# Kernel optimization log

Measured on AMD Instinct MI355X. Metric: run time of the kernel, lower is better.

Reference implementation:

```python
import jax, jax.numpy as jnp
import numpy as np

N = 20000   # nodes
E = 256000  # edges
G = 64      # graphs
EPS = 1e-5  # batchnorm eps


def setup_inputs() -> dict:
    key = jax.random.key(0)
    ks = jax.random.split(key, 20)
    inp = {}
    inp['x'] = jax.random.normal(ks[0], (N, 6), dtype=jnp.float32)
    inp['edge_index'] = jax.random.randint(ks[1], (2, E), 0, N)
    inp['batch'] = jnp.sort(jax.random.randint(ks[2], (N,), 0, G))
    conv_dims = [(6, 32), (32, 64), (64, 128), (128, 1024)]
    ki = 3
    for li, (a, b) in enumerate(conv_dims, 1):
        inp[f'W{li}'] = jax.random.normal(ks[ki], (a, b), dtype=jnp.float32) / np.sqrt(a).astype(np.float32); ki += 1
        inp[f'b{li}'] = jnp.zeros((b,), jnp.float32)
        inp[f'g{li}'] = jnp.ones((b,), jnp.float32)
        inp[f'be{li}'] = jnp.zeros((b,), jnp.float32)
    fc_dims = [(1024, 512), (512, 256), (256, 64)]
    for li, (a, b) in enumerate(fc_dims, 5):
        inp[f'W{li}'] = jax.random.normal(ks[ki], (a, b), dtype=jnp.float32) / np.sqrt(a).astype(np.float32); ki += 1
        inp[f'b{li}'] = jnp.zeros((b,), jnp.float32)
        if li < 7:
            inp[f'g{li}'] = jnp.ones((b,), jnp.float32)
            inp[f'be{li}'] = jnp.zeros((b,), jnp.float32)
    return inp


def _bn(h, g, be):
    # training-mode BatchNorm1d: biased variance over dim 0
    m = h.mean(axis=0)
    v = h.var(axis=0)
    return g * (h - m) * jax.lax.rsqrt(v + EPS) + be


def reference(x, edge_index, batch,
              W1, b1, g1, be1, W2, b2, g2, be2,
              W3, b3, g3, be3, W4, b4, g4, be4,
              W5, b5, g5, be5, W6, b6, g6, be6,
              W7, b7):
    loops = jnp.arange(N)
    src = jnp.concatenate([edge_index[0], loops])  # [E+N], message sources
    dst = jnp.concatenate([edge_index[1], loops])  # [E+N], aggregation targets
    deg = jax.ops.segment_sum(jnp.ones(E + N, x.dtype), dst, num_segments=N)
    dinv = jax.lax.rsqrt(deg)                      # deg >= 1 (self-loops)
    norm = dinv[src] * dinv[dst]                   # symmetric GCN normalization

    def gcn(h, W, b):
        h = h @ W                                   # [N, out]
        agg = jax.ops.segment_sum(norm[:, None] * h[src], dst, num_segments=N)
        return agg + b

    h = jax.nn.relu(_bn(gcn(x, W1, b1), g1, be1))
    h = jax.nn.relu(_bn(gcn(h, W2, b2), g2, be2))
    h = jax.nn.relu(_bn(gcn(h, W3, b3), g3, be3))
    h = jax.nn.relu(_bn(gcn(h, W4, b4), g4, be4))
    p = jax.ops.segment_max(h, batch, num_segments=G)  # global max pool [G, 1024]
    p = jax.nn.relu(_bn(p @ W5 + b5, g5, be5))
    p = jax.nn.relu(_bn(p @ W6 + b6, g6, be6))
    y = p @ W7 + b7
    n = jnp.maximum(jnp.linalg.norm(y, axis=1, keepdims=True), 1e-12)
    return y / n
```

## Files before the change

### kernel.cpp

```cpp
#include <hip/hip_runtime.h>
#include <math.h>

#define NN 20000
#define EE 256000
#define GG 64
#define CDIV(a,b) (((a)+(b)-1)/(b))

typedef __attribute__((ext_vector_type(8))) short bf16x8;
typedef __attribute__((ext_vector_type(4))) float f32x4;

__device__ __forceinline__ unsigned fkey(float f) {
  unsigned u = __float_as_uint(f);
  return (u & 0x80000000u) ? ~u : (u | 0x80000000u);
}
__device__ __forceinline__ float fdec(unsigned k) {
  unsigned u = (k & 0x80000000u) ? (k ^ 0x80000000u) : ~k;
  return __uint_as_float(u);
}
__device__ __forceinline__ unsigned short rne_bf16(float f) {
  unsigned u = __float_as_uint(f);
  unsigned r = (u + 0x7fffu + ((u >> 16) & 1u)) >> 16;
  return (unsigned short)r;
}


__global__ void k_prep(int* deg) {
  int i = blockIdx.x*blockDim.x + threadIdx.x;
  if (i < NN) deg[i] = 1;
}

__global__ void k_deg(const int* __restrict__ dst, int* deg) {
  int i = blockIdx.x*blockDim.x + threadIdx.x;
  if (i < EE) atomicAdd(&deg[dst[i]], 1);
}

__global__ __launch_bounds__(256) void k_scan_bsum(const int* __restrict__ deg,
                                                   int* __restrict__ bsum) {
  __shared__ int red[256];
  int b = blockIdx.x, t = threadIdx.x;
  int idx = b*1024 + t*4;
  int4 v = make_int4(0,0,0,0);
  if (idx < NN) v = *(const int4*)&deg[idx];
  red[t] = v.x + v.y + v.z + v.w;
  __syncthreads();
  for (int off = 128; off > 0; off >>= 1) {
    if (t < off) red[t] += red[t+off];
    __syncthreads();
  }
  if (t == 0) bsum[b] = red[0];
}

__global__ __launch_bounds__(256) void k_scan_apply(
    const int* __restrict__ deg, const int* __restrict__ bsum,
    int* __restrict__ offsets, int* __restrict__ cursor, float* __restrict__ dinv) {
  __shared__ int base_s;
  __shared__ int tsum[256];
  int b = blockIdx.x, t = threadIdx.x;
  if (t == 0) {
    int s = 0;
    for (int i = 0; i < b; ++i) s += bsum[i];
    base_s = s;
  }
  int idx = b*1024 + t*4;
  int4 v = make_int4(0,0,0,0);
  if (idx < NN) v = *(const int4*)&deg[idx];
  tsum[t] = v.x + v.y + v.z + v.w;
  __syncthreads();
  for (int off = 1; off < 256; off <<= 1) {
    int u = (t >= off) ? tsum[t-off] : 0;
    __syncthreads();
    tsum[t] += u;
    __syncthreads();
  }
  int excl = (t == 0) ? 0 : tsum[t-1];
  if (idx < NN) {
    int base = base_s + excl;
    int o0 = base;
    int o1 = o0 + v.x;
    int o2 = o1 + v.y;
    int o3 = o2 + v.z;
    *(int4*)&offsets[idx] = make_int4(o0,o1,o2,o3);
    *(int4*)&cursor[idx]  = make_int4(o0,o1,o2,o3);
    float4 dv;
    dv.x = rsqrtf((float)v.x); dv.y = rsqrtf((float)v.y);
    dv.z = rsqrtf((float)v.z); dv.w = rsqrtf((float)v.w);
    *(float4*)&dinv[idx] = dv;
    if (idx + 4 == NN) offsets[NN] = o3 + v.w;
  }
}

__global__ void k_fill(const int* __restrict__ srcv, const int* __restrict__ dstv,
                       const float* __restrict__ dinv, int* cursor,
                       int* __restrict__ csr_src, float* __restrict__ csr_w) {
  int i = blockIdx.x*blockDim.x + threadIdx.x;
  if (i < EE) {
    int s = srcv[i], d = dstv[i];
    int pos = atomicAdd(&cursor[d], 1);
    csr_src[pos] = s;
    csr_w[pos] = dinv[s] * dinv[d];
  } else if (i < EE + NN) {
    int n = i - EE;
    int pos = atomicAdd(&cursor[n], 1);
    csr_src[pos] = n;
    float di = dinv[n];
    csr_w[pos] = di * di;
  }
}


template<int C, int TX, int TY>
__global__ void k_agg(const float* __restrict__ in, const int* __restrict__ offsets,
                      const int* __restrict__ csr_src, const float* __restrict__ csr_w,
                      float* __restrict__ out) {
  int node = blockIdx.x * TY + threadIdx.y;
  if (node >= NN) return;
  int x = threadIdx.x;
  int k0 = offsets[node], k1 = offsets[node+1];
  if (x < C) {
    float acc = 0.f;
    for (int k = k0; k < k1; ++k) {
      int s = csr_src[k];
      float w = csr_w[k];
      acc += w * in[s*C + x];
    }
    out[node*C + x] = acc;
  }
}

template<int C, int TY>
__global__ void k_agg_f4(const float* __restrict__ in, const float* __restrict__ st,
                         const float* __restrict__ g, const float* __restrict__ be,
                         const int* __restrict__ offsets, const int* __restrict__ csr_src,
                         const float* __restrict__ csr_w, float* __restrict__ out) {
  int node = blockIdx.x*TY + threadIdx.y;
  if (node >= NN) return;
  int c0 = threadIdx.x*4;
  float4 mean = *(const float4*)&st[c0];
  float4 rstd = *(const float4*)&st[C+c0];
  float4 gv = *(const float4*)&g[c0];
  float4 bv = *(const float4*)&be[c0];
  float sx = gv.x*rstd.x, hx = bv.x - mean.x*sx;
  float sy = gv.y*rstd.y, hy = bv.y - mean.y*sy;
  float sz = gv.z*rstd.z, hz = bv.z - mean.z*sz;
  float sw = gv.w*rstd.w, hw = bv.w - mean.w*sw;
  int k0 = offsets[node], k1 = offsets[node+1];
  float a0=0.f,a1=0.f,a2=0.f,a3=0.f;
  for (int k = k0; k < k1; ++k) {
    int s = csr_src[k]; float w = csr_w[k];
    float4 v = *(const float4*)&in[s*C + c0];
    a0 += w*fmaxf(v.x*sx+hx, 0.f);
    a1 += w*fmaxf(v.y*sy+hy, 0.f);
    a2 += w*fmaxf(v.z*sz+hz, 0.f);
    a3 += w*fmaxf(v.w*sw+hw, 0.f);
  }
  *(float4*)&out[node*C+c0] = make_float4(a0,a1,a2,a3);
}

__global__ void k_agg_bf_f4(const float* __restrict__ in, const float* __restrict__ st,
                            const float* __restrict__ g, const float* __restrict__ be,
                            const int* __restrict__ offsets, const int* __restrict__ csr_src,
                            const float* __restrict__ csr_w, unsigned short* __restrict__ out) {
  int node = blockIdx.x*8 + threadIdx.y;
  if (node >= NN) return;
  int c0 = threadIdx.x*4;
  float4 mean = *(const float4*)&st[c0];
  float4 rstd = *(const float4*)&st[128+c0];
  float4 gv = *(const float4*)&g[c0];
  float4 bv = *(const float4*)&be[c0];
  float sx = gv.x*rstd.x, hx = bv.x - mean.x*sx;
  float sy = gv.y*rstd.y, hy = bv.y - mean.y*sy;
  float sz = gv.z*rstd.z, hz = bv.z - mean.z*sz;
  float sw = gv.w*rstd.w, hw = bv.w - mean.w*sw;
  int k0 = offsets[node], k1 = offsets[node+1];
  float a0=0.f,a1=0.f,a2=0.f,a3=0.f;
  for (int k = k0; k < k1; ++k) {
    int s = csr_src[k]; float w = csr_w[k];
    float4 v = *(const float4*)&in[s*128 + c0];
    a0 += w*fmaxf(v.x*sx+hx, 0.f);
    a1 += w*fmaxf(v.y*sy+hy, 0.f);
    a2 += w*fmaxf(v.z*sz+hz, 0.f);
    a3 += w*fmaxf(v.w*sw+hw, 0.f);
  }
  ushort4 o;
  o.x = rne_bf16(a0); o.y = rne_bf16(a1); o.z = rne_bf16(a2); o.w = rne_bf16(a3);
  *(ushort4*)&out[node*128 + c0] = o;
}

__global__ void k_wprep(const float* __restrict__ W, unsigned short* __restrict__ out) {
  int i = blockIdx.x*256 + threadIdx.x;
  if (i >= 128*1024) return;
  int k = i >> 10, c = i & 1023;
  out[c*128 + k] = rne_bf16(W[i]);
}


template<int K, int OUT, int ROWS>
__global__ __launch_bounds__(256) void k_gemm_small(
    const float* __restrict__ A, const float* __restrict__ W,
    float* __restrict__ out, float* __restrict__ pstats) {
  constexpr int RG  = 256 / OUT;
  constexpr int RPT = ROWS / RG;
  __shared__ float Ws[K*OUT];
  __shared__ float As[ROWS*K];
  __shared__ float reds[2][RG][OUT];
  int t = threadIdx.x;
  for (int i = t; i < K*OUT; i += 256) Ws[i] = W[i];
  int row0 = blockIdx.x * ROWS;
  for (int i = t; i < ROWS*K; i += 256) As[i] = A[row0*K + i];
  __syncthreads();
  int j  = t % OUT;
  int rg = t / OUT;
  float acc[RPT] = {};
  for (int k = 0; k < K; ++k) {
    float w = Ws[k*OUT + j];
    #pragma unroll
    for (int i = 0; i < RPT; ++i)
      acc[i] += As[(rg*RPT + i)*K + k] * w;
  }
  float s = 0.f, ss = 0.f;
  #pragma unroll
  for (int i = 0; i < RPT; ++i) {
    out[(row0 + rg*RPT + i)*OUT + j] = acc[i];
    s += acc[i]; ss += acc[i]*acc[i];
  }
  reds[0][rg][j] = s; reds[1][rg][j] = ss;
  __syncthreads();
  if (rg == 0) {
    float S = 0.f, SS = 0.f;
    #pragma unroll
    for (int r = 0; r < RG; ++r) { S += reds[0][r][j]; SS += reds[1][r][j]; }
    int p = blockIdx.x & 15;
    atomicAdd(&pstats[p*2*OUT + j], S);
    atomicAdd(&pstats[p*2*OUT + OUT + j], SS);
  }
}

template<int C>
__global__ void k_finalize_ps(const float* __restrict__ pstats, float* __restrict__ stats) {
  int c = blockIdx.x*64 + threadIdx.x;
  if (c >= C) return;
  float s = 0.f, ss = 0.f;
  #pragma unroll
  for (int p = 0; p < 16; ++p) { s += pstats[p*2*C + c]; ss += pstats[p*2*C + C + c]; }
  float m = s * (1.f/NN);
  float v = ss * (1.f/NN) - m*m;
  stats[c] = m;
  stats[C+c] = rsqrtf(v + 1e-5f);
}


__global__ __launch_bounds__(256) void k_gemm_l4_mfma(
    const unsigned short* __restrict__ A, const unsigned short* __restrict__ Bt,
    const int* __restrict__ batch,
    float* __restrict__ stats, unsigned* __restrict__ pmax, unsigned* __restrict__ pmin) {
  __shared__ unsigned short As[128*128];
  __shared__ unsigned short Bs[128*128];
  int t = threadIdx.x;
  int row0 = blockIdx.x * 128;
  int col0 = blockIdx.y * 128;
  #pragma unroll
  for (int j = 0; j < 8; ++j) {
    int c = j*256 + t;
    int r = c >> 4, ck = c & 15;
    int rg = row0 + r;
    ulonglong2 v; v.x = 0; v.y = 0;
    if (rg < NN) v = *(const ulonglong2*)&A[rg*128 + ck*8];
    *(ulonglong2*)&As[r*128 + (ck ^ (r & 7))*8] = v;
  }
  #pragma unroll
  for (int j = 0; j < 8; ++j) {
    int c = j*256 + t;
    int r = c >> 4, ck = c & 15;
    ulonglong2 v = *(const ulonglong2*)&Bt[(col0 + r)*128 + ck*8];
    *(ulonglong2*)&Bs[r*128 + (ck ^ (r & 7))*8] = v;
  }
  __syncthreads();

  int w = t >> 6, l = t & 63;
  int wr = w >> 1, wc = w & 1;
  int lrow = l & 15, lk = l >> 4;
  f32x4 acc[4][4] = {};
  #pragma unroll
  for (int ks = 0; ks < 4; ++ks) {
    int kc = ks*4 + lk;
    bf16x8 a[4], b[4];
    #pragma unroll
    for (int m = 0; m < 4; ++m) {
      int r = wr*64 + m*16 + lrow;
      a[m] = *(const bf16x8*)&As[r*128 + (kc ^ (r & 7))*8];
    }
    #pragma unroll
    for (int n = 0; n < 4; ++n) {
      int r = wc*64 + n*16 + lrow;
      b[n] = *(const bf16x8*)&Bs[r*128 + (kc ^ (r & 7))*8];
    }
    #pragma unroll
    for (int m = 0; m < 4; ++m)
      #pragma unroll
      for (int n = 0; n < 4; ++n)
        acc[m][n] = __builtin_amdgcn_mfma_f32_16x16x32_bf16(a[m], b[n], acc[m][n], 0, 0, 0);
  }

  int rbase = row0 + wr*64;
  float s[4] = {}, ss[4] = {};
  float mx[4], mn[4];
  #pragma unroll
  for (int n = 0; n < 4; ++n) { mx[n] = -3.4e38f; mn[n] = 3.4e38f; }
  #pragma unroll
  for (int m = 0; m < 4; ++m)
    #pragma unroll
    for (int r = 0; r < 4; ++r) {
      int row_g = rbase + m*16 + lk*4 + r;
      if (row_g < NN) {
        #pragma unroll
        for (int n = 0; n < 4; ++n) {
          float v = acc[m][n][r];
          s[n] += v; ss[n] += v*v;
          mx[n] = fmaxf(mx[n], v); mn[n] = fminf(mn[n], v);
        }
      }
    }
  #pragma unroll
  for (int n = 0; n < 4; ++n) {
    s[n]  += __shfl_xor(s[n], 16);  s[n]  += __shfl_xor(s[n], 32);
    ss[n] += __shfl_xor(ss[n], 16); ss[n] += __shfl_xor(ss[n], 32);
  }
  if (l < 16) {
    #pragma unroll
    for (int n = 0; n < 4; ++n) {
      int cg = col0 + wc*64 + n*16 + l;
      atomicAdd(&stats[cg], s[n]);
      atomicAdd(&stats[1024 + cg], ss[n]);
    }
  }
  if (rbase < NN) {
    int rlast = min(rbase + 63, NN - 1);
    int glo = batch[rbase], ghi = batch[rlast];
    if (glo == ghi) {
      #pragma unroll
      for (int n = 0; n < 4; ++n) {
        mx[n] = fmaxf(mx[n], __shfl_xor(mx[n], 16)); mx[n] = fmaxf(mx[n], __shfl_xor(mx[n], 32));
        mn[n] = fminf(mn[n], __shfl_xor(mn[n], 16)); mn[n] = fminf(mn[n], __shfl_xor(mn[n], 32));
      }
      if (l < 16) {
        #pragma unroll
        for (int n = 0; n < 4; ++n) {
          int cg = col0 + wc*64 + n*16 + l;
          atomicMax(&pmax[glo*1024 + cg], fkey(mx[n]));
          atomicMin(&pmin[glo*1024 + cg], fkey(mn[n]));
        }
      }
    } else {
      int gb[4][4];
      #pragma unroll
      for (int m = 0; m < 4; ++m)
        #pragma unroll
        for (int r = 0; r < 4; ++r) {
          int row_g = rbase + m*16 + lk*4 + r;
          gb[m][r] = (row_g < NN) ? batch[row_g] : -1;
        }
      for (int g = glo; g <= ghi; ++g) {
        float gmx[4], gmn[4];
        #pragma unroll
        for (int n = 0; n < 4; ++n) { gmx[n] = -3.4e38f; gmn[n] = 3.4e38f; }
        #pragma unroll
        for (int m = 0; m < 4; ++m)
          #pragma unroll
          for (int r = 0; r < 4; ++r) {
            bool in_g = (gb[m][r] == g);
            #pragma unroll
            for (int n = 0; n < 4; ++n) {
              float v = acc[m][n][r];
              gmx[n] = in_g ? fmaxf(gmx[n], v) : gmx[n];
              gmn[n] = in_g ? fminf(gmn[n], v) : gmn[n];
            }
          }
        #pragma unroll
        for (int n = 0; n < 4; ++n) {
          gmx[n] = fmaxf(gmx[n], __shfl_xor(gmx[n], 16)); gmx[n] = fmaxf(gmx[n], __shfl_xor(gmx[n], 32));
          gmn[n] = fminf(gmn[n], __shfl_xor(gmn[n], 16)); gmn[n] = fminf(gmn[n], __shfl_xor(gmn[n], 32));
        }
        if (l < 16) {
          #pragma unroll
          for (int n = 0; n < 4; ++n) {
            int cg = col0 + wc*64 + n*16 + l;
            if (gmx[n] > -3.0e38f) atomicMax(&pmax[g*1024 + cg], fkey(gmx[n]));
            if (gmn[n] <  3.0e38f) atomicMin(&pmin[g*1024 + cg], fkey(gmn[n]));
          }
        }
      }
    }
  }
}

__global__ void k_finalize(float* stats, int C, float invN) {
  int c = blockIdx.x*blockDim.x + threadIdx.x;
  if (c < C) {
    float m = stats[c] * invN;
    float v = stats[C+c]*invN - m*m;
    stats[c] = m;
    stats[C+c] = rsqrtf(v + 1e-5f);
  }
}

__global__ void k_bnpool(const unsigned* __restrict__ pmax, const unsigned* __restrict__ pmin,
                         const float* __restrict__ stats, const float* __restrict__ g,
                         const float* __restrict__ be, float* __restrict__ p) {
  int i = blockIdx.x*256 + threadIdx.x;
  if (i >= 64*1024) return;
  int c = i & 1023;
  float mean = stats[c], rstd = stats[1024+c];
  float sc = g[c]*rstd, sh = be[c] - mean*sc;
  float v = (sc >= 0.f) ? fdec(pmax[i]) : fdec(pmin[i]);
  p[i] = fmaxf(v*sc + sh, 0.f);
}


template<int K, int OUT, int KT>
__global__ __launch_bounds__(256) void k_fc_tile(
    const float* __restrict__ A, const float* __restrict__ W,
    float* __restrict__ out) {
  __shared__ float As[64][KT];
  __shared__ float Ws[KT][64];
  int t = threadIdx.y*64 + threadIdx.x;
  int j0 = blockIdx.x*64;
  int k0 = blockIdx.y*KT;
  #pragma unroll 4
  for (int i = t; i < 64*KT/4; i += 256) {
    int r  = i / (KT/4);
    int c4 = i % (KT/4);
    float4 v = *(const float4*)&A[r*K + k0 + c4*4];
    *(float4*)&As[r][c4*4] = v;
  }
  #pragma unroll 4
  for (int i = t; i < KT*16; i += 256) {
    int k  = i / 16;
    int c4 = i % 16;
    float4 v = *(const float4*)&W[(k0+k)*OUT + j0 + c4*4];
    *(float4*)&Ws[k][c4*4] = v;
  }
  __syncthreads();
  int j  = threadIdx.x;
  int r0 = threadIdx.y*16;
  float acc[16] = {};
  for (int kk = 0; kk < KT; ++kk) {
    float w = Ws[kk][j];
    #pragma unroll
    for (int i = 0; i < 16; ++i) acc[i] += As[r0+i][kk] * w;
  }
  #pragma unroll
  for (int i = 0; i < 16; ++i) atomicAdd(&out[(r0+i)*OUT + j0 + j], acc[i]);
}

__global__ __launch_bounds__(512) void k_bn_rows(
    float* __restrict__ h, const float* __restrict__ g,
    const float* __restrict__ be, int C) {
  int c = blockIdx.x*64 + threadIdx.x;
  int y = threadIdx.y;
  float v[8];
  float s = 0.f, ss = 0.f;
  #pragma unroll
  for (int i = 0; i < 8; ++i) {
    v[i] = h[(y*8+i)*C + c];
    s += v[i]; ss += v[i]*v[i];
  }
  __shared__ float rs[8][64], rss[8][64], bc[2][64];
  rs[y][threadIdx.x] = s; rss[y][threadIdx.x] = ss;
  __syncthreads();
  if (y == 0) {
    s = 0.f; ss = 0.f;
    #pragma unroll
    for (int i = 0; i < 8; ++i) { s += rs[i][threadIdx.x]; ss += rss[i][threadIdx.x]; }
    float m = s*(1.f/64.f);
    float var = ss*(1.f/64.f) - m*m;
    float rstd = rsqrtf(var + 1e-5f);
    float sc = g[c]*rstd;
    bc[0][threadIdx.x] = sc;
    bc[1][threadIdx.x] = be[c] - m*sc;
  }
  __syncthreads();
  float sc = bc[0][threadIdx.x], sh = bc[1][threadIdx.x];
  #pragma unroll
  for (int i = 0; i < 8; ++i)
    h[(y*8+i)*C + c] = fmaxf(v[i]*sc + sh, 0.f);
}

__global__ void k_l2norm(const float* __restrict__ in, const float* __restrict__ b,
                         float* __restrict__ out) {
  int r = blockIdx.x, j = threadIdx.x;
  float v = in[r*64 + j] + b[j];
  float ss = v*v;
  #pragma unroll
  for (int off = 1; off < 64; off <<= 1) ss += __shfl_xor(ss, off);
  float inv = 1.f / fmaxf(sqrtf(ss), 1e-12f);
  out[r*64 + j] = v * inv;
}


extern "C" void kernel_launch(void* const* d_in, const int* in_sizes, int n_in,
                              void* d_out, int out_size, void* d_ws, size_t ws_size,
                              hipStream_t stream) {
  const float* x    = (const float*)d_in[0];
  const int*   ei   = (const int*)d_in[1];
  const int*   batch= (const int*)d_in[2];
  const float* W1=(const float*)d_in[3],  *g1=(const float*)d_in[5],  *be1=(const float*)d_in[6];
  const float* W2=(const float*)d_in[7],  *g2=(const float*)d_in[9],  *be2=(const float*)d_in[10];
  const float* W3=(const float*)d_in[11], *g3=(const float*)d_in[13], *be3=(const float*)d_in[14];
  const float* W4=(const float*)d_in[15], *g4=(const float*)d_in[17], *be4=(const float*)d_in[18];
  const float* W5=(const float*)d_in[19], *g5=(const float*)d_in[21], *be5=(const float*)d_in[22];
  const float* W6=(const float*)d_in[23], *g6=(const float*)d_in[25], *be6=(const float*)d_in[26];
  const float* W7=(const float*)d_in[27], *b7=(const float*)d_in[28];
  const int* esrc = ei;
  const int* edst = ei + EE;

  char* w = (char*)d_ws;
  auto alloc = [&](size_t bytes) -> void* {
    void* p = (void*)w;
    w += (bytes + 255) & ~(size_t)255;
    return p;
  };
  int*   deg     = (int*)  alloc(NN*4);
  int*   offsets = (int*)  alloc((NN+1)*4);
  int*   cursor  = (int*)  alloc(NN*4);
  int*   bsum    = (int*)  alloc(32*4);
  float* dinv    = (float*)alloc(NN*4);
  int*   csr_src = (int*)  alloc((EE+NN)*4);
  float* csr_w   = (float*)alloc((EE+NN)*4);
  float* stats1  = (float*)alloc(2*32*4);
  float* stats2  = (float*)alloc(2*64*4);
  float* stats3  = (float*)alloc(2*128*4);
  float* stats4  = (float*)alloc(2*1024*4);
  float* pstats  = (float*)alloc(16*2*128*4);
  float* agg     = (float*)alloc((size_t)NN*128*4);
  float* hbufA   = (float*)alloc((size_t)NN*128*4);
  float* hbufB   = (float*)alloc((size_t)NN*64*4);
  float* pooled  = (float*)alloc(64*1024*4);
  float* fc1     = (float*)alloc(64*512*4);
  float* fc2     = (float*)alloc(64*256*4);
  float* fc3raw  = (float*)alloc(64*64*4);
  unsigned short* agg_bf = (unsigned short*)alloc((size_t)NN*128*2);
  unsigned short* wt_bf  = (unsigned short*)alloc(1024*128*2);
  unsigned* pmax = (unsigned*)alloc(64*1024*4);
  unsigned* pmin = (unsigned*)alloc(64*1024*4);

  k_prep<<<CDIV(NN,256),256,0,stream>>>(deg);
  k_deg<<<CDIV(EE,256),256,0,stream>>>(edst, deg);
  k_scan_bsum<<<20,256,0,stream>>>(deg, bsum);
  k_scan_apply<<<20,256,0,stream>>>(deg, bsum, offsets, cursor, dinv);
  k_fill<<<CDIV(EE+NN,256),256,0,stream>>>(esrc, edst, dinv, cursor, csr_src, csr_w);

  k_agg<6,8,32><<<CDIV(NN,32),dim3(8,32),0,stream>>>(x, offsets, csr_src, csr_w, agg);
  hipMemsetAsync(pstats, 0, 16*2*32*4, stream);
  k_gemm_small<6,32,32><<<NN/32,256,0,stream>>>(agg, W1, hbufA, pstats);
  k_finalize_ps<32><<<1,64,0,stream>>>(pstats, stats1);

  k_agg_f4<32,32><<<CDIV(NN,32),dim3(8,32),0,stream>>>(hbufA, stats1, g1, be1, offsets, csr_src, csr_w, agg);
  hipMemsetAsync(pstats, 0, 16*2*64*4, stream);
  k_gemm_small<32,64,16><<<NN/16,256,0,stream>>>(agg, W2, hbufB, pstats);
  k_finalize_ps<64><<<1,64,0,stream>>>(pstats, stats2);

  k_agg_f4<64,16><<<CDIV(NN,16),dim3(16,16),0,stream>>>(hbufB, stats2, g2, be2, offsets, csr_src, csr_w, agg);
  hipMemsetAsync(pstats, 0, 16*2*128*4, stream);
  k_gemm_small<64,128,16><<<NN/16,256,0,stream>>>(agg, W3, hbufA, pstats);
  k_finalize_ps<128><<<2,64,0,stream>>>(pstats, stats3);

  k_agg_bf_f4<<<CDIV(NN,8),dim3(32,8),0,stream>>>(hbufA, stats3, g3, be3, offsets, csr_src, csr_w, agg_bf);
  k_wprep<<<CDIV(128*1024,256),256,0,stream>>>(W4, wt_bf);
  hipMemsetAsync(stats4, 0, 2*1024*4, stream);
  hipMemsetAsync(pmax, 0x00, 64*1024*4, stream);
  hipMemsetAsync(pmin, 0xFF, 64*1024*4, stream);
  k_gemm_l4_mfma<<<dim3(CDIV(NN,128),8),256,0,stream>>>(agg_bf, wt_bf, batch, stats4, pmax, pmin);
  k_finalize<<<4,256,0,stream>>>(stats4, 1024, 1.f/NN);
  k_bnpool<<<CDIV(64*1024,256),256,0,stream>>>(pmax, pmin, stats4, g4, be4, pooled);

  hipMemsetAsync(fc1, 0, 64*512*4, stream);
  k_fc_tile<1024,512,128><<<dim3(8,8),dim3(64,4),0,stream>>>(pooled, W5, fc1);
  k_bn_rows<<<8,dim3(64,8),0,stream>>>(fc1, g5, be5, 512);

  hipMemsetAsync(fc2, 0, 64*256*4, stream);
  k_fc_tile<512,256,128><<<dim3(4,4),dim3(64,4),0,stream>>>(fc1, W6, fc2);
  k_bn_rows<<<4,dim3(64,8),0,stream>>>(fc2, g6, be6, 256);

  hipMemsetAsync(fc3raw, 0, 64*64*4, stream);
  k_fc_tile<256,64,64><<<dim3(1,4),dim3(64,4),0,stream>>>(fc2, W7, fc3raw);
  k_l2norm<<<64,64,0,stream>>>(fc3raw, b7, (float*)d_out);
}
```

Before: 346.6 us.

## Replace layer-4 stats atomics with per-block partials and block-level pool reduction

The layer-4 MFMA GEMM epilogue now merges its two row-waves through shared memory. Each row block writes per-column sum and sum-of-squares partials to a buffer instead of doing global atomicAdds. When all 128 rows of a block belong to one graph, max/min pooling is reduced across the block first, which halves the pooling atomics. A new finalize kernel sums the 157 partial rows, and the stats memset is dropped. The cost is extra __syncthreads, shared-memory reuse, and a serial 157-step reduction in the finalize kernel.

```diff
diff --git a/kernel.cpp b/kernel.cpp
--- a/kernel.cpp
+++ b/kernel.cpp
@@ -5,6 +5,7 @@
 #define EE 256000
 #define GG 64
 #define CDIV(a,b) (((a)+(b)-1)/(b))
+#define RB4 157
 
 typedef __attribute__((ext_vector_type(8))) short bf16x8;
 typedef __attribute__((ext_vector_type(4))) float f32x4;
@@ -252,7 +253,7 @@
 __global__ __launch_bounds__(256) void k_gemm_l4_mfma(
     const unsigned short* __restrict__ A, const unsigned short* __restrict__ Bt,
     const int* __restrict__ batch,
-    float* __restrict__ stats, unsigned* __restrict__ pmax, unsigned* __restrict__ pmin) {
+    float* __restrict__ ps4, unsigned* __restrict__ pmax, unsigned* __restrict__ pmin) {
   __shared__ unsigned short As[128*128];
   __shared__ unsigned short Bs[128*128];
   int t = threadIdx.x;
@@ -325,15 +326,48 @@
     s[n]  += __shfl_xor(s[n], 16);  s[n]  += __shfl_xor(s[n], 32);
     ss[n] += __shfl_xor(ss[n], 16); ss[n] += __shfl_xor(ss[n], 32);
   }
+
+  int rlast_b = min(row0 + 127, NN - 1);
+  int glo_b = batch[row0], ghi_b = batch[rlast_b];
+  bool block_same = (glo_b == ghi_b);
+  if (block_same) {
+    #pragma unroll
+    for (int n = 0; n < 4; ++n) {
+      mx[n] = fmaxf(mx[n], __shfl_xor(mx[n], 16)); mx[n] = fmaxf(mx[n], __shfl_xor(mx[n], 32));
+      mn[n] = fminf(mn[n], __shfl_xor(mn[n], 16)); mn[n] = fminf(mn[n], __shfl_xor(mn[n], 32));
+    }
+  }
+
+  __syncthreads();
+  float* scr_s = (float*)As;
+  float* scr_p = (float*)Bs;
   if (l < 16) {
     #pragma unroll
     for (int n = 0; n < 4; ++n) {
-      int cg = col0 + wc*64 + n*16 + l;
-      atomicAdd(&stats[cg], s[n]);
-      atomicAdd(&stats[1024 + cg], ss[n]);
-    }
-  }
-  if (rbase < NN) {
+      int si = (((wr*2 + wc)*4 + n)*16 + l)*2;
+      scr_s[si]   = s[n];
+      scr_s[si+1] = ss[n];
+      if (block_same) { scr_p[si] = mx[n]; scr_p[si+1] = mn[n]; }
+    }
+  }
+  __syncthreads();
+  if (wr == 0 && l < 16) {
+    #pragma unroll
+    for (int n = 0; n < 4; ++n) {
+      int si0 = (((0*2 + wc)*4 + n)*16 + l)*2;
+      int si1 = (((1*2 + wc)*4 + n)*16 + l)*2;
+      int cg  = col0 + wc*64 + n*16 + l;
+      ps4[(size_t)blockIdx.x*2048 + cg]        = scr_s[si0]   + scr_s[si1];
+      ps4[(size_t)blockIdx.x*2048 + 1024 + cg] = scr_s[si0+1] + scr_s[si1+1];
+      if (block_same) {
+        float bmx = fmaxf(scr_p[si0],   scr_p[si1]);
+        float bmn = fminf(scr_p[si0+1], scr_p[si1+1]);
+        if (bmx > -3.0e38f) atomicMax(&pmax[glo_b*1024 + cg], fkey(bmx));
+        if (bmn <  3.0e38f) atomicMin(&pmin[glo_b*1024 + cg], fkey(bmn));
+      }
+    }
+  }
+  if (!block_same && rbase < NN) {
     int rlast = min(rbase + 63, NN - 1);
     int glo = batch[rbase], ghi = batch[rlast];
     if (glo == ghi) {
@@ -393,14 +427,18 @@
   }
 }
 
-__global__ void k_finalize(float* stats, int C, float invN) {
-  int c = blockIdx.x*blockDim.x + threadIdx.x;
-  if (c < C) {
-    float m = stats[c] * invN;
-    float v = stats[C+c]*invN - m*m;
-    stats[c] = m;
-    stats[C+c] = rsqrtf(v + 1e-5f);
-  }
+__global__ void k_finalize_l4(const float* __restrict__ ps4, float* __restrict__ stats) {
+  int c = blockIdx.x*256 + threadIdx.x;
+  float s = 0.f, ss = 0.f;
+  #pragma unroll 8
+  for (int rb = 0; rb < RB4; ++rb) {
+    s  += ps4[(size_t)rb*2048 + c];
+    ss += ps4[(size_t)rb*2048 + 1024 + c];
+  }
+  float m = s * (1.f/NN);
+  float v = ss * (1.f/NN) - m*m;
+  stats[c] = m;
+  stats[1024 + c] = rsqrtf(v + 1e-5f);
 }
 
 __global__ void k_bnpool(const unsigned* __restrict__ pmax, const unsigned* __restrict__ pmin,
@@ -531,6 +569,7 @@
   float* stats3  = (float*)alloc(2*128*4);
   float* stats4  = (float*)alloc(2*1024*4);
   float* pstats  = (float*)alloc(16*2*128*4);
+  float* ps4     = (float*)alloc((size_t)RB4*2048*4);
   float* agg     = (float*)alloc((size_t)NN*128*4);
   float* hbufA   = (float*)alloc((size_t)NN*128*4);
   float* hbufB   = (float*)alloc((size_t)NN*64*4);
@@ -566,11 +605,10 @@
 
   k_agg_bf_f4<<<CDIV(NN,8),dim3(32,8),0,stream>>>(hbufA, stats3, g3, be3, offsets, csr_src, csr_w, agg_bf);
   k_wprep<<<CDIV(128*1024,256),256,0,stream>>>(W4, wt_bf);
-  hipMemsetAsync(stats4, 0, 2*1024*4, stream);
   hipMemsetAsync(pmax, 0x00, 64*1024*4, stream);
   hipMemsetAsync(pmin, 0xFF, 64*1024*4, stream);
-  k_gemm_l4_mfma<<<dim3(CDIV(NN,128),8),256,0,stream>>>(agg_bf, wt_bf, batch, stats4, pmax, pmin);
-  k_finalize<<<4,256,0,stream>>>(stats4, 1024, 1.f/NN);
+  k_gemm_l4_mfma<<<dim3(RB4,8),256,0,stream>>>(agg_bf, wt_bf, batch, ps4, pmax, pmin);
+  k_finalize_l4<<<4,256,0,stream>>>(ps4, stats4);
   k_bnpool<<<CDIV(64*1024,256),256,0,stream>>>(pmax, pmin, stats4, g4, be4, pooled);
 
   hipMemsetAsync(fc1, 0, 64*512*4, stream);
```

Result: slower. 357.4 us (+3.1%).
